# Optimization experiments

Hardware: AMD Instinct MI355X
Metric: run time of the kernel (lower is better)

The kernel has to match this reference:

```python
import jax, jax.numpy as jnp
import numpy as np

T = 32          # timesteps
GAIN = 1.0      # input_gain
TAU = 2.0       # LIF membrane time constant
VTH = 1.0       # v_threshold
VRESET = 0.0    # v_reset (hard reset)
ALPHA = 2.0     # ATan surrogate alpha


@jax.custom_vjp
def heaviside_atan(x):
    # forward: Heaviside spike; backward: ATan surrogate gradient
    return (x >= 0).astype(x.dtype)

def _hs_fwd(x):
    return heaviside_atan(x), x

def _hs_bwd(x, g):
    # d/dx ATan surrogate: (alpha/2) / (1 + (pi/2 * alpha * x)^2)
    return (g * (ALPHA / 2.0) / (1.0 + (jnp.pi / 2.0 * ALPHA * x) ** 2),)

heaviside_atan.defvjp(_hs_fwd, _hs_bwd)


def lif_multistep(cur_seq):
    """Multi-step LIF over cur_seq [T, B, H]; hard reset, detach_reset=True."""
    def step(v, x):
        # charge: v = v + (x - (v - v_reset)) / tau
        v = v + (x - (v - VRESET)) / TAU
        spike = heaviside_atan(v - VTH)
        sd = jax.lax.stop_gradient(spike)  # detach_reset
        v = (1.0 - sd) * v + sd * VRESET   # hard reset
        return v, spike

    v0 = jnp.full(cur_seq.shape[1:], VRESET, dtype=cur_seq.dtype)
    _, spikes = jax.lax.scan(step, v0, cur_seq)
    return spikes


def setup_inputs() -> dict:
    key = jax.random.key(0)
    ks = jax.random.split(key, 4)

    def xavier(k, o, i):
        lim = np.sqrt(6.0 / (i + o)).astype(np.float32)
        return jax.random.uniform(k, (o, i), minval=-lim, maxval=lim, dtype=jnp.float32)

    x_flat = jax.random.uniform(ks[0], (512, 784), dtype=jnp.float32)
    W0 = xavier(ks[1], 1024, 784)
    b0 = jnp.zeros((1024,), jnp.float32)
    W1 = xavier(ks[2], 1024, 1024)
    b1 = jnp.zeros((1024,), jnp.float32)
    W2 = xavier(ks[3], 10, 1024)
    b2 = jnp.zeros((10,), jnp.float32)
    return {"x_flat": x_flat, "W0": W0, "b0": b0, "W1": W1, "b1": b1, "W2": W2, "b2": b2}


def reference(x_flat, W0, b0, W1, b1, W2, b2):
    # repeat_static_input: [B, 784] -> [T, B, 784]
    h = jnp.broadcast_to(x_flat * GAIN, (T,) + x_flat.shape)
    count = None
    for W, b in ((W0, b0), (W1, b1), (W2, b2)):
        cur = jnp.einsum('tbi,oi->tbo', h, W) + b  # fc over all timesteps
        spk = lif_multistep(cur)                   # [T, B, out]
        count = spk.sum(axis=0)                    # spike counts [B, out]
        h = spk
    # predict() returns argmax(count); return the final count (logits) here
    return count
```

## Files before the change

### kernel.cpp

```cpp
#include <hip/hip_runtime.h>
#include <hip/hip_bf16.h>
#include <stdint.h>


typedef __bf16 bf16x8 __attribute__((ext_vector_type(8)));
typedef float  f32x4  __attribute__((ext_vector_type(4)));

__device__ __forceinline__ void gload16(const void* g, void* l) {
  __builtin_amdgcn_global_load_lds((const __attribute__((address_space(1))) void*)g,
                                   (__attribute__((address_space(3))) void*)l,
                                   16, 0, 0);
}

__device__ __forceinline__ void bsplit3(float v, __hip_bfloat16& h,
                                        __hip_bfloat16& m, __hip_bfloat16& l) {
  h = __float2bfloat16(v);
  float r1 = v - __bfloat162float(h);
  m = __float2bfloat16(r1);
  float r2 = r1 - __bfloat162float(m);
  l = __float2bfloat16(r2);
}

__global__ __launch_bounds__(256) void prep_k(const float* __restrict__ x,
                                              const float* __restrict__ W0,
                                              __hip_bfloat16* __restrict__ Ax,
                                              __hip_bfloat16* __restrict__ Bw) {
  const int bid = blockIdx.x, tid = threadIdx.x;
  if (bid < 1600) {
    int i = bid * 256 + tid;
    int m = i / 800, k = i - m * 800;
    float v = (k < 784) ? x[(size_t)m * 784 + k] : 0.f;
    __hip_bfloat16 h, mm, l;
    bsplit3(v, h, mm, l);
    size_t base = (size_t)m * 4800;
    Ax[base + k] = h;         Ax[base + 800 + k] = h;
    Ax[base + 1600 + k] = mm; Ax[base + 2400 + k] = mm;
    Ax[base + 3200 + k] = h;  Ax[base + 4000 + k] = l;
  } else {
    int i = (bid - 1600) * 256 + tid;
    int n = i / 800, k = i - n * 800;
    float v = (k < 784) ? W0[(size_t)n * 784 + k] : 0.f;
    __hip_bfloat16 h, mm, l;
    bsplit3(v, h, mm, l);
    size_t base = (size_t)n * 4800;
    Bw[base + k] = h;         Bw[base + 800 + k] = mm;
    Bw[base + 1600 + k] = h;  Bw[base + 2400 + k] = mm;
    Bw[base + 3200 + k] = l;  Bw[base + 4000 + k] = h;
  }
}

__global__ __launch_bounds__(256, 2) void gemm0t_k(const __hip_bfloat16* __restrict__ A,
                                                   const __hip_bfloat16* __restrict__ B,
                                                   const float* __restrict__ W1,
                                                   float* __restrict__ W1T,
                                                   float* __restrict__ Cpart) {
  __shared__ __align__(16) char smem[16384];
  const int bid = blockIdx.x, tid = threadIdx.x;

  if (bid >= 320) {
    float (*t)[33] = (float(*)[33])smem;
    int tt = bid - 320;
    int c0 = (tt & 31) * 32, r0 = (tt >> 5) * 32;
    int lx = tid & 31, ly = tid >> 5;
#pragma unroll
    for (int i = 0; i < 32; i += 8)
      t[ly + i][lx] = W1[(size_t)(r0 + ly + i) * 1024 + (c0 + lx)];
    __syncthreads();
#pragma unroll
    for (int i = 0; i < 32; i += 8)
      W1T[(size_t)(c0 + ly + i) * 1024 + (r0 + lx)] = t[lx][ly + i];
    return;
  }

  __hip_bfloat16* As = (__hip_bfloat16*)smem;
  __hip_bfloat16* Bs = As + 128 * 32;
  const int bx = bid & 3, by = (bid >> 2) & 7, bz = bid >> 5;
  const int wave = tid >> 6, lane = tid & 63, quad = lane >> 4, l16 = lane & 15;
  const int wm = (wave >> 1) * 64, wn = (wave & 1) * 64;
  const int mbase = bx * 128, nbase = by * 128, kbase = bz * 480;
  const int srow = lane >> 2;
  const int gq = (lane & 3) ^ ((lane >> 3) & 3);
  const int swz = (l16 >> 1) & 3;
  f32x4 acc[4][4] = {};
  for (int kk = kbase; kk < kbase + 480; kk += 32) {
#pragma unroll
    for (int r = 0; r < 2; ++r) {
      int grp = wave * 2 + r;
      gload16(A + (size_t)(mbase + grp * 16 + srow) * 4800 + kk + gq * 8,
              (char*)As + grp * 1024);
      gload16(B + (size_t)(nbase + grp * 16 + srow) * 4800 + kk + gq * 8,
              (char*)Bs + grp * 1024);
    }
    __syncthreads();
    const __bf16* Ab = (const __bf16*)As;
    const __bf16* Bb = (const __bf16*)Bs;
    bf16x8 af[4], bfr[4];
#pragma unroll
    for (int i = 0; i < 4; ++i)
      af[i] = *(const bf16x8*)(Ab + (wm + i * 16 + l16) * 32 + ((quad ^ swz) * 8));
#pragma unroll
    for (int j = 0; j < 4; ++j)
      bfr[j] = *(const bf16x8*)(Bb + (wn + j * 16 + l16) * 32 + ((quad ^ swz) * 8));
#pragma unroll
    for (int i = 0; i < 4; ++i)
#pragma unroll
      for (int j = 0; j < 4; ++j)
        acc[i][j] = __builtin_amdgcn_mfma_f32_16x16x32_bf16(af[i], bfr[j], acc[i][j], 0, 0, 0);
    __syncthreads();
  }
  float* Cz = Cpart + (size_t)bz * 512 * 1024;
#pragma unroll
  for (int i = 0; i < 4; ++i)
#pragma unroll
    for (int j = 0; j < 4; ++j)
#pragma unroll
      for (int r = 0; r < 4; ++r) {
        int m = mbase + wm + i * 16 + quad * 4 + r;
        int n = nbase + wn + j * 16 + l16;
        Cz[(size_t)m * 1024 + n] = acc[i][j][r];
      }
}

struct TailSM {
  unsigned short sidx[1024];
  int sseg[33];
  int mtot;
  unsigned l2i[1024];
  unsigned l2w[1024];
  union {
    struct { int whist[16][33]; int clstot[33]; int clsofs[34]; int wofs[16][33]; } s3;
    struct { int wtot[16]; int wbase[16]; } s4;
    struct { float sW2[10 * 1025]; float scur[320]; } s5;
  } u;
};

__global__ __launch_bounds__(1024) void tail_k(const float* __restrict__ Cpart,
                                               const float* __restrict__ b0,
                                               const float* __restrict__ W1T,
                                               const float* __restrict__ b1,
                                               const float* __restrict__ W2,
                                               const float* __restrict__ b2,
                                               float* __restrict__ out) {
  __shared__ TailSM sm;
  const int b = blockIdx.x, o = threadIdx.x;
  const int wave = o >> 6, lane = o & 63;

  {
    float cur = 0.f;
#pragma unroll
    for (int z = 0; z < 10; ++z)
      cur += Cpart[(size_t)z * 512 * 1024 + (size_t)b * 1024 + o];
    cur += b0[o];
    float v = 0.f;
    unsigned word = 0u;
#pragma unroll
    for (int t = 0; t < 32; ++t) {
      v = v + (cur - v) * 0.5f;
      if (v >= 1.0f) { word |= 1u << t; v = 0.f; }
    }
    int n = word ? (__builtin_ctz(word) + 1) : 0;
    unsigned long long mymask = 0ull;
#pragma unroll 1
    for (int c = 1; c <= 32; ++c) {
      unsigned long long m = __ballot(n == c);
      if (lane == 0) sm.u.s3.whist[wave][c] = __popcll(m);
      if (n == c) mymask = m;
    }
    __syncthreads();
    if (o < 32) {
      int c = o + 1, s = 0;
#pragma unroll
      for (int w = 0; w < 16; ++w) s += sm.u.s3.whist[w][c];
      sm.u.s3.clstot[c] = s;
    }
    __syncthreads();
    if (o == 0) {
      int run = 0;
#pragma unroll
      for (int c = 1; c <= 32; ++c) { sm.u.s3.clsofs[c] = run; run += sm.u.s3.clstot[c]; }
      sm.u.s3.clsofs[33] = run;
    }
    __syncthreads();
    if (o < 32) {
      int c = o + 1, s = sm.u.s3.clsofs[c];
#pragma unroll
      for (int w = 0; w < 16; ++w) { sm.u.s3.wofs[w][c] = s; s += sm.u.s3.whist[w][c]; }
    }
    __syncthreads();
    if (n) {
      int pos = sm.u.s3.wofs[wave][n] + __popcll(mymask & ((1ull << lane) - 1ull));
      sm.sidx[pos] = (unsigned short)o;
    }
    if (o < 33) sm.sseg[o] = sm.u.s3.clsofs[o + 1];
  }
  __syncthreads();

  {
    float S[32];
#pragma unroll
    for (int c = 0; c < 32; ++c) {
      int j0 = __builtin_amdgcn_readfirstlane((c == 0) ? 0 : sm.sseg[c - 1]);
      int j1 = __builtin_amdgcn_readfirstlane(sm.sseg[c]);
      float s = 0.f;
      for (int j = j0; j < j1; ++j)
        s += W1T[(size_t)sm.sidx[j] * 1024 + o];
      S[c] = s;
    }
    const float bias = b1[o];
    float v = 0.f;
    unsigned word = 0u;
#pragma unroll
    for (int t = 0; t < 32; ++t) {
      float cur = 0.f;
#pragma unroll
      for (int c = 1; c <= 32; ++c)
        if ((t + 1) % c == 0) cur += S[c - 1];
      float xc = cur + bias;
      v = v + (xc - v) * 0.5f;
      if (v >= 1.0f) { word |= 1u << t; v = 0.f; }
    }
    bool act = (word != 0u);
    unsigned long long m = __ballot(act);
    if (lane == 0) sm.u.s4.wtot[wave] = __popcll(m);
    __syncthreads();
    if (o == 0) {
      int s = 0;
#pragma unroll
      for (int i = 0; i < 16; ++i) { sm.u.s4.wbase[i] = s; s += sm.u.s4.wtot[i]; }
      sm.mtot = s;
    }
    __syncthreads();
    if (act) {
      int pos = sm.u.s4.wbase[wave] + __popcll(m & ((1ull << lane) - 1ull));
      sm.l2i[pos] = (unsigned)o;
      sm.l2w[pos] = word;
    }
  }
  __syncthreads();

  {
    for (int i = o; i < 10240; i += 1024)
      sm.u.s5.sW2[(i >> 10) * 1025 + (i & 1023)] = W2[i];
    __syncthreads();
    const int mtot = sm.mtot;
    if (o < 320) {
      int t = o / 10, c = o - t * 10;
      float acc = 0.f;
      for (int j = 0; j < mtot; ++j) {
        unsigned wd = sm.l2w[j];
        float wv = sm.u.s5.sW2[c * 1025 + sm.l2i[j]];
        acc += ((wd >> t) & 1u) ? wv : 0.f;
      }
      sm.u.s5.scur[o] = acc;
    }
    __syncthreads();
    if (o < 10) {
      float v = 0.f, cnt2 = 0.f, bias = b2[o];
#pragma unroll
      for (int tt = 0; tt < 32; ++tt) {
        float xc = sm.u.s5.scur[tt * 10 + o] + bias;
        v = v + (xc - v) * 0.5f;
        if (v >= 1.0f) { cnt2 += 1.f; v = 0.f; }
      }
      out[(size_t)b * 10 + o] = cnt2;
    }
  }
}

extern "C" void kernel_launch(void* const* d_in, const int* in_sizes, int n_in,
                              void* d_out, int out_size, void* d_ws, size_t ws_size,
                              hipStream_t stream) {
  const float* x  = (const float*)d_in[0];
  const float* W0 = (const float*)d_in[1];
  const float* b0 = (const float*)d_in[2];
  const float* W1 = (const float*)d_in[3];
  const float* b1 = (const float*)d_in[4];
  const float* W2 = (const float*)d_in[5];
  const float* b2 = (const float*)d_in[6];
  float* out = (float*)d_out;

  char* ws = (char*)d_ws;
  size_t off = 0;
  auto alloc = [&](size_t bytes) -> char* {
    char* p = ws + off;
    off += (bytes + 255) & ~(size_t)255;
    return p;
  };
  __hip_bfloat16* Ax    = (__hip_bfloat16*)alloc((size_t)512 * 4800 * 2);
  __hip_bfloat16* Bw    = (__hip_bfloat16*)alloc((size_t)1024 * 4800 * 2);
  float*          Cpart = (float*)alloc((size_t)10 * 512 * 1024 * 4);
  float*          W1T   = (float*)alloc((size_t)1024 * 1024 * 4);
  (void)ws_size;

  prep_k<<<4800, 256, 0, stream>>>(x, W0, Ax, Bw);
  gemm0t_k<<<1344, 256, 0, stream>>>(Ax, Bw, W1, W1T, Cpart);
  tail_k<<<512, 1024, 0, stream>>>(Cpart, b0, W1T, b1, W2, b2, out);
}
```

Measured before the change: 111.3 us.

## Store 3-way bf16 split once and shrink GEMM0 tiles to 64x64

The prep kernel now writes each bf16 split component (hi, mid, lo) once per row instead of duplicating them into a 6-segment K layout. The GEMM picks segment offsets per K chunk through small offset tables. The GEMM tile also drops from 128x128 to 64x64 with 2x2 MFMA per wave, giving 1280 GEMM blocks instead of 320. This halves the prep write traffic and the workspace size, and raises block-level parallelism. In exchange, each block reuses less data from LDS and issues more global loads per MFMA.

Result: no change. 111.5 us (+0.1%).

```diff
diff --git a/kernel.cpp b/kernel.cpp
--- a/kernel.cpp
+++ b/kernel.cpp
@@ -32,20 +32,20 @@
     float v = (k < 784) ? x[(size_t)m * 784 + k] : 0.f;
     __hip_bfloat16 h, mm, l;
     bsplit3(v, h, mm, l);
-    size_t base = (size_t)m * 4800;
-    Ax[base + k] = h;         Ax[base + 800 + k] = h;
-    Ax[base + 1600 + k] = mm; Ax[base + 2400 + k] = mm;
-    Ax[base + 3200 + k] = h;  Ax[base + 4000 + k] = l;
+    size_t base = (size_t)m * 2400;
+    Ax[base + k] = h;
+    Ax[base + 800 + k] = mm;
+    Ax[base + 1600 + k] = l;
   } else {
     int i = (bid - 1600) * 256 + tid;
     int n = i / 800, k = i - n * 800;
     float v = (k < 784) ? W0[(size_t)n * 784 + k] : 0.f;
     __hip_bfloat16 h, mm, l;
     bsplit3(v, h, mm, l);
-    size_t base = (size_t)n * 4800;
-    Bw[base + k] = h;         Bw[base + 800 + k] = mm;
-    Bw[base + 1600 + k] = h;  Bw[base + 2400 + k] = mm;
-    Bw[base + 3200 + k] = l;  Bw[base + 4000 + k] = h;
+    size_t base = (size_t)n * 2400;
+    Bw[base + k] = h;
+    Bw[base + 800 + k] = mm;
+    Bw[base + 1600 + k] = l;
   }
 }
 
@@ -54,12 +54,12 @@
                                                    const float* __restrict__ W1,
                                                    float* __restrict__ W1T,
                                                    float* __restrict__ Cpart) {
-  __shared__ __align__(16) char smem[16384];
+  __shared__ __align__(16) char smem[8192];
   const int bid = blockIdx.x, tid = threadIdx.x;
 
-  if (bid >= 320) {
+  if (bid >= 1280) {
     float (*t)[33] = (float(*)[33])smem;
-    int tt = bid - 320;
+    int tt = bid - 1280;
     int c0 = (tt & 31) * 32, r0 = (tt >> 5) * 32;
     int lx = tid & 31, ly = tid >> 5;
 #pragma unroll
@@ -73,46 +73,48 @@
   }
 
   __hip_bfloat16* As = (__hip_bfloat16*)smem;
-  __hip_bfloat16* Bs = As + 128 * 32;
-  const int bx = bid & 3, by = (bid >> 2) & 7, bz = bid >> 5;
+  __hip_bfloat16* Bs = As + 64 * 32;
+  const int bx = bid & 7, by = (bid >> 3) & 15, bz = bid >> 7;
   const int wave = tid >> 6, lane = tid & 63, quad = lane >> 4, l16 = lane & 15;
-  const int wm = (wave >> 1) * 64, wn = (wave & 1) * 64;
-  const int mbase = bx * 128, nbase = by * 128, kbase = bz * 480;
+  const int wm = (wave >> 1) * 32, wn = (wave & 1) * 32;
+  const int mbase = bx * 64, nbase = by * 64, kbase = bz * 480;
   const int srow = lane >> 2;
   const int gq = (lane & 3) ^ ((lane >> 3) & 3);
   const int swz = (l16 >> 1) & 3;
-  f32x4 acc[4][4] = {};
+  const int offA[6] = {0, 0, 800, 800, 0, 1600};
+  const int offB[6] = {0, 800, 0, 800, 1600, 0};
+
+  f32x4 acc[2][2] = {};
+
   for (int kk = kbase; kk < kbase + 480; kk += 32) {
-#pragma unroll
-    for (int r = 0; r < 2; ++r) {
-      int grp = wave * 2 + r;
-      gload16(A + (size_t)(mbase + grp * 16 + srow) * 4800 + kk + gq * 8,
-              (char*)As + grp * 1024);
-      gload16(B + (size_t)(nbase + grp * 16 + srow) * 4800 + kk + gq * 8,
-              (char*)Bs + grp * 1024);
-    }
-    __syncthreads();
-    const __bf16* Ab = (const __bf16*)As;
-    const __bf16* Bb = (const __bf16*)Bs;
-    bf16x8 af[4], bfr[4];
-#pragma unroll
-    for (int i = 0; i < 4; ++i)
-      af[i] = *(const bf16x8*)(Ab + (wm + i * 16 + l16) * 32 + ((quad ^ swz) * 8));
-#pragma unroll
-    for (int j = 0; j < 4; ++j)
-      bfr[j] = *(const bf16x8*)(Bb + (wn + j * 16 + l16) * 32 + ((quad ^ swz) * 8));
-#pragma unroll
-    for (int i = 0; i < 4; ++i)
-#pragma unroll
-      for (int j = 0; j < 4; ++j)
+    const int s = kk / 800;
+    const int kloc = kk - s * 800;
+    const int kA = kloc + offA[s], kB = kloc + offB[s];
+    gload16(A + (size_t)(mbase + wave * 16 + srow) * 2400 + kA + gq * 8,
+            (char*)As + wave * 1024);
+    gload16(B + (size_t)(nbase + wave * 16 + srow) * 2400 + kB + gq * 8,
+            (char*)Bs + wave * 1024);
+    __syncthreads();
+    bf16x8 af[2], bfr[2];
+#pragma unroll
+    for (int i = 0; i < 2; ++i)
+      af[i] = *(const bf16x8*)((const __bf16*)As + (wm + i * 16 + l16) * 32 + ((quad ^ swz) * 8));
+#pragma unroll
+    for (int j = 0; j < 2; ++j)
+      bfr[j] = *(const bf16x8*)((const __bf16*)Bs + (wn + j * 16 + l16) * 32 + ((quad ^ swz) * 8));
+#pragma unroll
+    for (int i = 0; i < 2; ++i)
+#pragma unroll
+      for (int j = 0; j < 2; ++j)
         acc[i][j] = __builtin_amdgcn_mfma_f32_16x16x32_bf16(af[i], bfr[j], acc[i][j], 0, 0, 0);
     __syncthreads();
   }
+
   float* Cz = Cpart + (size_t)bz * 512 * 1024;
 #pragma unroll
-  for (int i = 0; i < 4; ++i)
-#pragma unroll
-    for (int j = 0; j < 4; ++j)
+  for (int i = 0; i < 2; ++i)
+#pragma unroll
+    for (int j = 0; j < 2; ++j)
 #pragma unroll
       for (int r = 0; r < 4; ++r) {
         int m = mbase + wm + i * 16 + quad * 4 + r;
@@ -286,13 +288,13 @@
     off += (bytes + 255) & ~(size_t)255;
     return p;
   };
-  __hip_bfloat16* Ax    = (__hip_bfloat16*)alloc((size_t)512 * 4800 * 2);
-  __hip_bfloat16* Bw    = (__hip_bfloat16*)alloc((size_t)1024 * 4800 * 2);
+  __hip_bfloat16* Ax    = (__hip_bfloat16*)alloc((size_t)512 * 2400 * 2);
+  __hip_bfloat16* Bw    = (__hip_bfloat16*)alloc((size_t)1024 * 2400 * 2);
   float*          Cpart = (float*)alloc((size_t)10 * 512 * 1024 * 4);
   float*          W1T   = (float*)alloc((size_t)1024 * 1024 * 4);
   (void)ws_size;
 
   prep_k<<<4800, 256, 0, stream>>>(x, W0, Ax, Bw);
-  gemm0t_k<<<1344, 256, 0, stream>>>(Ax, Bw, W1, W1T, Cpart);
+  gemm0t_k<<<2304, 256, 0, stream>>>(Ax, Bw, W1, W1T, Cpart);
   tail_k<<<512, 1024, 0, stream>>>(Cpart, b0, W1T, b1, W2, b2, out);
 }
```
